# Kernel tuning notes

Hardware: AMD Instinct MI355X
Metric: run time of the kernel (lower is better)

Reference implementation:

```python
import jax, jax.numpy as jnp
import numpy as np

LN_EPS = 1e-5


def setup_inputs() -> dict:
    key = jax.random.key(0)
    ks = jax.random.split(key, 12)
    B, T, C, D, P = 4, 1024, 16, 256, 4096
    s = 1.0 / np.sqrt(D)
    x = jax.random.normal(ks[0], (B, T, C, D), jnp.float32)
    x_mask = jax.random.uniform(ks[1], (B, T, C)) < 0.1
    pos = jax.random.randint(ks[2], (B, T, C), 0, P)
    ang = jax.random.uniform(ks[3], (P, D // 2), minval=-np.pi, maxval=np.pi)
    pe = jnp.stack([jnp.cos(ang), jnp.sin(ang)], axis=-1)  # [P, D/2, 2] unit complex
    wq_w = jax.random.normal(ks[4], (D, D), jnp.float32) * s
    wq_b = jnp.zeros((D,), jnp.float32)
    wk_w = jax.random.normal(ks[5], (D, D), jnp.float32) * s
    wk_b = jnp.zeros((D,), jnp.float32)
    wv_w = jax.random.normal(ks[6], (D, D), jnp.float32) * s
    wv_b = jnp.zeros((D,), jnp.float32)
    ln_g = jnp.ones((D,), jnp.float32)
    ln_b = jnp.zeros((D,), jnp.float32)
    ls_gamma = 1e-5 * jnp.ones((D,), jnp.float32)
    return {"x": x, "x_mask": x_mask, "pos": pos, "pe": pe,
            "wq_w": wq_w, "wq_b": wq_b, "wk_w": wk_w, "wk_b": wk_b,
            "wv_w": wv_w, "wv_b": wv_b, "ln_g": ln_g, "ln_b": ln_b,
            "ls_gamma": ls_gamma}


def _rotate(q, pe, pos):
    # q: [B,T,C,D]; pe: [P,D/2,2]; pos: [B,T,C] -> complex mult q * pe[pos]
    B, T, C, D = q.shape
    qr = q.reshape(B, T, C, D // 2, 2)
    r = pe[pos]  # [B,T,C,D/2,2]
    re = qr[..., 0] * r[..., 0] - qr[..., 1] * r[..., 1]
    im = qr[..., 0] * r[..., 1] + qr[..., 1] * r[..., 0]
    return jnp.stack([re, im], axis=-1).reshape(B, T, C, D)


def reference(x, x_mask, pos, pe, wq_w, wq_b, wk_w, wk_b, wv_w, wv_b, ln_g, ln_b, ls_gamma):
    B, T, C, D = x.shape
    scale = 1.0 / jnp.sqrt(jnp.asarray(D, x.dtype))
    q = jnp.einsum('btcd,ed->btce', x, wq_w) + wq_b
    k = jnp.einsum('btcd,ed->btce', x, wk_w) + wk_b
    v = jnp.einsum('btcd,ed->btce', x, wv_w) + wv_b
    q = _rotate(q, pe, pos)
    k = _rotate(k, pe, pos)
    # (b c) t d layout -> keep as [b,c,t,d]
    q = q.transpose(0, 2, 1, 3)
    k = k.transpose(0, 2, 1, 3)
    v = v.transpose(0, 2, 1, 3)
    attn = jnp.einsum('bcqd,bckd->bcqk', q, k) * scale  # [b,c,tq,tk]
    m = x_mask.transpose(0, 2, 1)  # [b,c,t]
    mask = m[:, :, :, None] | m[:, :, None, :]  # OR-combined pad mask
    attn = jnp.where(mask, jnp.asarray(-1e30, attn.dtype), attn)
    p = jax.nn.softmax(attn, axis=-1)
    # fully masked rows: torch softmax(-inf row)->nan->nan_to_num(0)
    all_masked = jnp.all(mask, axis=-1, keepdims=True)
    p = jnp.where(all_masked, jnp.zeros((), p.dtype), p)
    o = jnp.einsum('bcqk,bckd->bqcd', p, v)  # [b,t,c,d]
    y = x + ls_gamma * o
    mu = y.mean(-1, keepdims=True)
    var = ((y - mu) ** 2).mean(-1, keepdims=True)
    out = (y - mu) / jnp.sqrt(var + LN_EPS) * ln_g + ln_b
    return out
```

## Files before the change

### kernel.cpp

```cpp
#include <hip/hip_runtime.h>


typedef __attribute__((ext_vector_type(8))) short short8_t;
typedef __attribute__((ext_vector_type(4))) short short4_t;
typedef __attribute__((ext_vector_type(8))) float float8_t;
typedef __attribute__((ext_vector_type(4))) float float4_t;
typedef __attribute__((ext_vector_type(2))) float float2_t;

__device__ __forceinline__ float b2f(short s) {
    union { unsigned int u; float f; } x;
    x.u = ((unsigned int)(unsigned short)s) << 16;
    return x.f;
}
__device__ __forceinline__ short f2bt(float f) {
    union { float f; unsigned int u; } x; x.f = f;
    return (short)(x.u >> 16);
}

__device__ __forceinline__ void stage16(const short* g, short* l) {
    __builtin_amdgcn_global_load_lds(
        (const __attribute__((address_space(1))) unsigned int*)g,
        (__attribute__((address_space(3))) unsigned int*)l, 16, 0, 0);
}

__global__ __launch_bounds__(256) void prep_kernel(
    const float* __restrict__ wq, const float* __restrict__ wk,
    const float* __restrict__ wv, const unsigned char* __restrict__ xmask,
    short* __restrict__ wb, float* __restrict__ mbg)
{
    if (blockIdx.x < 192) {
        int idx = blockIdx.x * 256 + threadIdx.x;
        int mat = idx >> 14, off = idx & 16383;
        const float* src = (mat == 0) ? wq : ((mat == 1) ? wk : wv);
        float4_t v = *(const float4_t*)(src + (long)off * 4);
        short4_t o;
#pragma unroll
        for (int j = 0; j < 4; j++) o[j] = f2bt(v[j]);
        *(short4_t*)(wb + (long)idx * 4) = o;
    } else {
        int idx = (blockIdx.x - 192) * 256 + threadIdx.x;
        int bc = idx >> 10, t = idx & 1023;
        int b = bc >> 4, c = bc & 15;
        mbg[idx] = xmask[((long)b * 1024 + t) * 16 + c] ? -1e30f : 0.0f;
    }
}

__global__ __launch_bounds__(256) void qkv_mfma_kernel(
    const float* __restrict__ x, const int* __restrict__ pos,
    const float* __restrict__ pe, const short* __restrict__ wb,
    const float* __restrict__ bq, const float* __restrict__ bk,
    const float* __restrict__ bv,
    short* __restrict__ qo, short* __restrict__ ko, short* __restrict__ vt)
{
    __shared__ __align__(16) short xs[64 * 264];
    __shared__ __align__(16) short ys[18432];
    __shared__ int posb[64];

    const int tid = threadIdx.x;
    const int lane = tid & 63;
    const int wid = tid >> 6;
    const int bc = blockIdx.x >> 4;
    const int t0 = (blockIdx.x & 15) * 64;
    const int b = bc >> 4, c = bc & 15;
    const int row = lane & 15, quad = lane >> 4;
    const int odd = lane & 1;
    const int n0 = wid * 64;
    const long kvbase = (long)bc * 262144;

#pragma unroll
    for (int j = 0; j < 8; j++) {
        int idx = tid + j * 256;
        int r = idx >> 5, c8 = idx & 31;
        const float* xp = x + (((long)b * 1024 + t0 + r) * 16 + c) * 256 + c8 * 8;
        float4_t a = *(const float4_t*)xp;
        float4_t d = *(const float4_t*)(xp + 4);
        short8_t o;
        o[0] = f2bt(a.x); o[1] = f2bt(a.y); o[2] = f2bt(a.z); o[3] = f2bt(a.w);
        o[4] = f2bt(d.x); o[5] = f2bt(d.y); o[6] = f2bt(d.z); o[7] = f2bt(d.w);
        *(short8_t*)&xs[r * 264 + c8 * 8] = o;
    }
    if (tid < 64) posb[tid] = pos[((long)b * 1024 + t0 + tid) * 16 + c];
    __syncthreads();

#pragma unroll 1
    for (int mat = 0; mat < 3; mat++) {
        const short* W = wb + mat * 65536;
        float4_t acc[4][4];
#pragma unroll
        for (int mt = 0; mt < 4; mt++)
#pragma unroll
            for (int nt = 0; nt < 4; nt++) acc[mt][nt] = (float4_t){0.f, 0.f, 0.f, 0.f};

        short8_t Ac[4], Bc[4], An[4], Bn[4];
        auto loadA = [&](short8_t* A, int k0) {
#pragma unroll
            for (int mt = 0; mt < 4; mt++)
                A[mt] = *(const short8_t*)&xs[(mt * 16 + row) * 264 + k0 * 32 + quad * 8];
        };
        auto loadB = [&](short8_t* Bf, int k0) {
#pragma unroll
            for (int nt = 0; nt < 4; nt++)
                Bf[nt] = *(const short8_t*)(W + (n0 + nt * 16 + row) * 256 + k0 * 32 + quad * 8);
        };
        loadA(Ac, 0); loadB(Bc, 0);
#pragma unroll
        for (int k0 = 0; k0 < 8; k0++) {
            if (k0 < 7) { loadA(An, k0 + 1); loadB(Bn, k0 + 1); }
#pragma unroll
            for (int mt = 0; mt < 4; mt++)
#pragma unroll
                for (int nt = 0; nt < 4; nt++)
                    acc[mt][nt] = __builtin_amdgcn_mfma_f32_16x16x32_bf16(
                        Ac[mt], Bc[nt], acc[mt][nt], 0, 0, 0);
            if (k0 < 7) {
#pragma unroll
                for (int i = 0; i < 4; i++) { Ac[i] = An[i]; Bc[i] = Bn[i]; }
            }
        }

        const float* bias = (mat == 0) ? bq : ((mat == 1) ? bk : bv);
        float bs[4];
#pragma unroll
        for (int nt = 0; nt < 4; nt++) bs[nt] = bias[n0 + nt * 16 + row];
#pragma unroll
        for (int mt = 0; mt < 4; mt++)
#pragma unroll
            for (int nt = 0; nt < 4; nt++)
#pragma unroll
                for (int r = 0; r < 4; r++) acc[mt][nt][r] += bs[nt];

        if (mat < 2) {
#pragma unroll
            for (int mt = 0; mt < 4; mt++)
#pragma unroll
                for (int r = 0; r < 4; r++) {
                    int p = posb[mt * 16 + quad * 4 + r];
                    const float* pb = pe + (long)p * 256;
#pragma unroll
                    for (int nt = 0; nt < 4; nt++) {
                        int i = (n0 + nt * 16 + row) >> 1;
                        float2_t cs = *(const float2_t*)(pb + i * 2);
                        float v = acc[mt][nt][r];
                        float pr = __shfl_xor(v, 1);
                        acc[mt][nt][r] = v * cs.x + pr * (odd ? cs.y : -cs.y);
                    }
                }
        }

        __syncthreads();
        if (mat < 2) {
#pragma unroll
            for (int mt = 0; mt < 4; mt++)
#pragma unroll
                for (int nt = 0; nt < 4; nt++) {
                    int n = n0 + nt * 16 + row;
#pragma unroll
                    for (int r = 0; r < 4; r++)
                        ys[(mt * 16 + quad * 4 + r) * 264 + n] = f2bt(acc[mt][nt][r]);
                }
            __syncthreads();
            short* dst = ((mat == 0) ? qo : ko) + kvbase + (long)t0 * 256;
#pragma unroll
            for (int j = 0; j < 8; j++) {
                int idx = tid + j * 256;
                int r = idx >> 5, c8 = idx & 31;
                *(short8_t*)(dst + r * 256 + c8 * 8) = *(const short8_t*)&ys[r * 264 + c8 * 8];
            }
        } else {
#pragma unroll
            for (int mt = 0; mt < 4; mt++)
#pragma unroll
                for (int nt = 0; nt < 4; nt++) {
                    int n = n0 + nt * 16 + row;
                    short4_t o4;
#pragma unroll
                    for (int r = 0; r < 4; r++) o4[r] = f2bt(acc[mt][nt][r]);
                    *(short4_t*)&ys[n * 72 + mt * 16 + quad * 4] = o4;
                }
            __syncthreads();
#pragma unroll
            for (int j = 0; j < 8; j++) {
                int idx = tid + j * 256;
                int d = idx >> 3, t8 = idx & 7;
                *(short8_t*)(vt + kvbase + (long)d * 1024 + t0 + t8 * 8) =
                    *(const short8_t*)&ys[d * 72 + t8 * 8];
            }
        }
    }
}

__global__ __launch_bounds__(512, 2) void attn_kernel(
    const short* __restrict__ qg, const short* __restrict__ kg,
    const short* __restrict__ vt, const float* __restrict__ mbg,
    const float* __restrict__ x,
    const float* __restrict__ lsg, const float* __restrict__ lng,
    const float* __restrict__ lnb, float* __restrict__ out)
{
    __shared__ __align__(16) short lds[72704];

    const int tid = threadIdx.x;
    const int lane = tid & 63;
    const int wid = tid >> 6;
    const int bid = (blockIdx.x & 7) * 64 + (blockIdx.x >> 3);
    const int bc = bid >> 3;
    const int tq0 = (bid & 7) * 128;
    const int b = bc >> 4, c = bc & 15;
    const long kvbase = (long)bc * 262144;
    const int bcq = bc * 1024;
    const int row = lane & 15, quad = lane >> 4;
    float* mbsf = (float*)&lds[70656];

    auto stage = [&](int j, int buf) {
#pragma unroll
        for (int i = 0; i < 2; i++) {
            int rp = (wid * 2 + i) * 2;
            int r = rp + (lane >> 5);
            int slot = lane & 31;
            const short* g = kg + kvbase + (long)(j * 32 + r) * 256 +
                             ((slot ^ (r & 7)) << 3);
            stage16(g, &lds[buf * 8192 + rp * 256]);
        }
#pragma unroll
        for (int i = 0; i < 2; i++) {
            int db = (wid * 2 + i) * 16;
            int d = db + (lane >> 2);
            int slot = lane & 3;
            const short* g = vt + kvbase + (long)d * 1024 + j * 32 +
                             (((slot ^ ((d >> 1) & 3))) << 3);
            stage16(g, &lds[32768 + buf * 8192 + db * 32]);
        }
    };

    stage(0, 0);
    stage(1, 1);
#pragma unroll
    for (int i = tid; i < 1024; i += 512) mbsf[i] = mbg[bcq + i];
    short8_t aq[8];
#pragma unroll
    for (int f = 0; f < 8; f++)
        aq[f] = *(const short8_t*)(qg + kvbase +
            (long)(tq0 + wid * 16 + row) * 256 + f * 32 + quad * 8);

    float4_t oacc[16];
#pragma unroll
    for (int nt = 0; nt < 16; nt++) oacc[nt] = (float4_t){0.f, 0.f, 0.f, 0.f};
    float m[4], lsum[4];
#pragma unroll
    for (int r = 0; r < 4; r++) { m[r] = -__builtin_inff(); lsum[r] = 0.f; }

    const float scale = 0.0625f;
    const int ptw = 65536 + wid * 640 + row * 20 + quad * 4;
    const int prd = 65536 + wid * 640 + quad * 160 + row;

    asm volatile("s_waitcnt lgkmcnt(0)" ::: "memory");

#pragma unroll 1
    for (int j = 0; j < 32; j++) {
        if (j < 30) {
            stage(j + 2, (j + 2) & 3);
            asm volatile("s_waitcnt vmcnt(8)" ::: "memory");
        } else if (j == 30) {
            asm volatile("s_waitcnt vmcnt(4)" ::: "memory");
        } else {
            asm volatile("s_waitcnt vmcnt(0)" ::: "memory");
        }
        __builtin_amdgcn_s_barrier();

        const short* Kb = &lds[(j & 3) * 8192];
        const short* Vb = &lds[32768 + (j & 3) * 8192];

        float4_t s0 = {0.f, 0.f, 0.f, 0.f}, s1 = {0.f, 0.f, 0.f, 0.f};
        __builtin_amdgcn_s_setprio(1);
#pragma unroll
        for (int f = 0; f < 8; f++) {
            short8_t k0 = *(const short8_t*)&Kb[row * 256 + (((f * 4 + quad) ^ (row & 7)) << 3)];
            short8_t k1 = *(const short8_t*)&Kb[(16 + row) * 256 + (((f * 4 + quad) ^ ((16 + row) & 7)) << 3)];
            s0 = __builtin_amdgcn_mfma_f32_16x16x32_bf16(aq[f], k0, s0, 0, 0, 0);
            s1 = __builtin_amdgcn_mfma_f32_16x16x32_bf16(aq[f], k1, s1, 0, 0, 0);
        }
        __builtin_amdgcn_s_setprio(0);
        float mb0 = mbsf[j * 32 + row], mb1 = mbsf[j * 32 + 16 + row];
        float sv[2][4], tm[4];
#pragma unroll
        for (int r = 0; r < 4; r++) {
            sv[0][r] = s0[r] * scale + mb0;
            sv[1][r] = s1[r] * scale + mb1;
            tm[r] = fmaxf(sv[0][r], sv[1][r]);
        }
#pragma unroll
        for (int r = 0; r < 4; r++)
#pragma unroll
            for (int o = 1; o < 16; o <<= 1) tm[r] = fmaxf(tm[r], __shfl_xor(tm[r], o));
        float g = fmaxf(fmaxf(tm[0] - m[0], tm[1] - m[1]),
                        fmaxf(tm[2] - m[2], tm[3] - m[3]));
        if (!__all(g <= 8.f)) {
#pragma unroll
            for (int r = 0; r < 4; r++) {
                float nm = fmaxf(m[r], tm[r]);
                float fac = __expf(m[r] - nm);
                lsum[r] *= fac; m[r] = nm;
#pragma unroll
                for (int nt = 0; nt < 16; nt++) oacc[nt][r] *= fac;
            }
        }
        short4_t p4[2];
#pragma unroll
        for (int h = 0; h < 2; h++)
#pragma unroll
            for (int r = 0; r < 4; r++) {
                float p = __expf(sv[h][r] - m[r]);
                lsum[r] += p;
                p4[h][r] = f2bt(p);
            }
        *(short4_t*)&lds[ptw] = p4[0];
        *(short4_t*)&lds[ptw + 320] = p4[1];
        short8_t pa;
#pragma unroll
        for (int jj = 0; jj < 8; jj++) pa[jj] = lds[prd + jj * 20];

        __builtin_amdgcn_s_setprio(1);
#pragma unroll
        for (int nt = 0; nt < 16; nt++) {
            int d = nt * 16 + row;
            short8_t vbf = *(const short8_t*)&Vb[d * 32 + ((quad ^ ((d >> 1) & 3)) << 3)];
            oacc[nt] = __builtin_amdgcn_mfma_f32_16x16x32_bf16(pa, vbf, oacc[nt], 0, 0, 0);
        }
        __builtin_amdgcn_s_setprio(0);
    }

    float inv[4];
#pragma unroll
    for (int r = 0; r < 4; r++) {
        float s = lsum[r];
#pragma unroll
        for (int o = 1; o < 16; o <<= 1) s += __shfl_xor(s, o);
        int qi = tq0 + wid * 16 + quad * 4 + r;
        inv[r] = (mbsf[qi] != 0.f) ? 0.f : (1.f / s);
    }
    long xb[4];
#pragma unroll
    for (int r = 0; r < 4; r++)
        xb[r] = (((long)b * 1024 + tq0 + wid * 16 + quad * 4 + r) * 16 + c) * 256 + row;

    float s1r[4] = {0.f, 0.f, 0.f, 0.f}, s2r[4] = {0.f, 0.f, 0.f, 0.f};
#pragma unroll
    for (int nt = 0; nt < 16; nt++) {
        int d = nt * 16 + row;
        float lg = lsg[d];
#pragma unroll
        for (int r = 0; r < 4; r++) {
            float yy = x[xb[r] + nt * 16] + lg * (oacc[nt][r] * inv[r]);
            oacc[nt][r] = yy;
            s1r[r] += yy; s2r[r] += yy * yy;
        }
    }
    float mu[4], rstd[4];
#pragma unroll
    for (int r = 0; r < 4; r++) {
#pragma unroll
        for (int o = 1; o < 16; o <<= 1) {
            s1r[r] += __shfl_xor(s1r[r], o);
            s2r[r] += __shfl_xor(s2r[r], o);
        }
        mu[r] = s1r[r] * (1.f / 256.f);
        float var = s2r[r] * (1.f / 256.f) - mu[r] * mu[r];
        rstd[r] = rsqrtf(var + 1e-5f);
    }
#pragma unroll
    for (int nt = 0; nt < 16; nt++) {
        int d = nt * 16 + row;
        float g2 = lng[d], b2 = lnb[d];
#pragma unroll
        for (int r = 0; r < 4; r++)
            out[xb[r] + nt * 16] = (oacc[nt][r] - mu[r]) * rstd[r] * g2 + b2;
    }
}

extern "C" void kernel_launch(void* const* d_in, const int* in_sizes, int n_in,
                              void* d_out, int out_size, void* d_ws, size_t ws_size,
                              hipStream_t stream) {
    const float* x = (const float*)d_in[0];
    const unsigned char* xmask = (const unsigned char*)d_in[1];
    const int* pos = (const int*)d_in[2];
    const float* pe = (const float*)d_in[3];
    const float* wq = (const float*)d_in[4];
    const float* bq = (const float*)d_in[5];
    const float* wk = (const float*)d_in[6];
    const float* bk = (const float*)d_in[7];
    const float* wv = (const float*)d_in[8];
    const float* bv = (const float*)d_in[9];
    const float* lng = (const float*)d_in[10];
    const float* lnb = (const float*)d_in[11];
    const float* lsg = (const float*)d_in[12];
    float* out = (float*)d_out;

    short* qw = (short*)d_ws;
    short* kw = qw + 16777216;
    short* vtw = kw + 16777216;
    short* wbw = vtw + 16777216;
    float* mbg = (float*)(wbw + 196608);

    prep_kernel<<<448, 256, 0, stream>>>(wq, wk, wv, xmask, wbw, mbg);
    qkv_mfma_kernel<<<1024, 256, 0, stream>>>(x, pos, pe, wbw, bq, bk, bv,
                                              qw, kw, vtw);
    attn_kernel<<<512, 512, 0, stream>>>(qw, kw, vtw, mbg, x, lsg, lng, lnb, out);
}
```

Before: 347.9 us.

## Switch attention to 32x32x16 MFMA with 256-query blocks and permlane P transpose

The attention kernel now gives each wave 32 query rows instead of 16 and uses 32x32x16 bf16 MFMA for both QK^T (computed transposed as K·Q) and PV. The P tile is rearranged into the A-operand layout with permlane32_swap instead of an LDS write/read round-trip, and each query's softmax state is kept per lane. Each block covers 256 queries, which halves the grid and doubles K/V reuse per LDS stage. The cost is higher register pressure (16 Q fragments and 8 float16 accumulators) and only 256 blocks, which may not fill the device at two blocks per CU.

```diff
diff --git a/kernel.cpp b/kernel.cpp
--- a/kernel.cpp
+++ b/kernel.cpp
@@ -5,7 +5,9 @@
 typedef __attribute__((ext_vector_type(4))) short short4_t;
 typedef __attribute__((ext_vector_type(8))) float float8_t;
 typedef __attribute__((ext_vector_type(4))) float float4_t;
+typedef __attribute__((ext_vector_type(16))) float float16_t;
 typedef __attribute__((ext_vector_type(2))) float float2_t;
+typedef __attribute__((ext_vector_type(2))) int int2_t;
 
 __device__ __forceinline__ float b2f(short s) {
     union { unsigned int u; float f; } x;
@@ -196,19 +198,20 @@
     const float* __restrict__ lsg, const float* __restrict__ lng,
     const float* __restrict__ lnb, float* __restrict__ out)
 {
-    __shared__ __align__(16) short lds[72704];
+    __shared__ __align__(16) short lds[68096];
 
     const int tid = threadIdx.x;
     const int lane = tid & 63;
     const int wid = tid >> 6;
-    const int bid = (blockIdx.x & 7) * 64 + (blockIdx.x >> 3);
-    const int bc = bid >> 3;
-    const int tq0 = (bid & 7) * 128;
+    const int bid = (blockIdx.x & 7) * 32 + (blockIdx.x >> 3);
+    const int bc = bid >> 2;
+    const int tq0 = (bid & 3) * 256;
     const int b = bc >> 4, c = bc & 15;
     const long kvbase = (long)bc * 262144;
     const int bcq = bc * 1024;
-    const int row = lane & 15, quad = lane >> 4;
-    float* mbsf = (float*)&lds[70656];
+    const int col = lane & 31, hi = lane >> 5;
+    float* mbsf = (float*)&lds[65536];
+    float* facb = (float*)&lds[67584];
 
     auto stage = [&](int j, int buf) {
 #pragma unroll
@@ -235,22 +238,24 @@
     stage(1, 1);
 #pragma unroll
     for (int i = tid; i < 1024; i += 512) mbsf[i] = mbg[bcq + i];
-    short8_t aq[8];
-#pragma unroll
-    for (int f = 0; f < 8; f++)
-        aq[f] = *(const short8_t*)(qg + kvbase +
-            (long)(tq0 + wid * 16 + row) * 256 + f * 32 + quad * 8);
-
-    float4_t oacc[16];
-#pragma unroll
-    for (int nt = 0; nt < 16; nt++) oacc[nt] = (float4_t){0.f, 0.f, 0.f, 0.f};
-    float m[4], lsum[4];
-#pragma unroll
-    for (int r = 0; r < 4; r++) { m[r] = -__builtin_inff(); lsum[r] = 0.f; }
+    short8_t aq[16];
+    {
+        const short* qrow = qg + kvbase + (long)(tq0 + wid * 32 + col) * 256;
+#pragma unroll
+        for (int f = 0; f < 16; f++)
+            aq[f] = *(const short8_t*)(qrow + f * 16 + hi * 8);
+    }
+
+    float16_t oacc[8];
+#pragma unroll
+    for (int nt = 0; nt < 8; nt++)
+#pragma unroll
+        for (int i = 0; i < 16; i++) oacc[nt][i] = 0.f;
+    float m = -__builtin_inff(), lsum = 0.f;
 
     const float scale = 0.0625f;
-    const int ptw = 65536 + wid * 640 + row * 20 + quad * 4;
-    const int prd = 65536 + wid * 640 + quad * 160 + row;
+    const int ksw = col & 7;
+    const int vsw = (col >> 1) & 3;
 
     asm volatile("s_waitcnt lgkmcnt(0)" ::: "memory");
 
@@ -269,110 +274,119 @@
         const short* Kb = &lds[(j & 3) * 8192];
         const short* Vb = &lds[32768 + (j & 3) * 8192];
 
-        float4_t s0 = {0.f, 0.f, 0.f, 0.f}, s1 = {0.f, 0.f, 0.f, 0.f};
+        float16_t s;
+#pragma unroll
+        for (int i = 0; i < 16; i++) s[i] = 0.f;
         __builtin_amdgcn_s_setprio(1);
 #pragma unroll
-        for (int f = 0; f < 8; f++) {
-            short8_t k0 = *(const short8_t*)&Kb[row * 256 + (((f * 4 + quad) ^ (row & 7)) << 3)];
-            short8_t k1 = *(const short8_t*)&Kb[(16 + row) * 256 + (((f * 4 + quad) ^ ((16 + row) & 7)) << 3)];
-            s0 = __builtin_amdgcn_mfma_f32_16x16x32_bf16(aq[f], k0, s0, 0, 0, 0);
-            s1 = __builtin_amdgcn_mfma_f32_16x16x32_bf16(aq[f], k1, s1, 0, 0, 0);
+        for (int f = 0; f < 16; f++) {
+            short8_t kf = *(const short8_t*)
+                &Kb[col * 256 + ((((f << 1) + hi) ^ ksw) << 3)];
+            s = __builtin_amdgcn_mfma_f32_32x32x16_bf16(kf, aq[f], s, 0, 0, 0);
         }
         __builtin_amdgcn_s_setprio(0);
-        float mb0 = mbsf[j * 32 + row], mb1 = mbsf[j * 32 + 16 + row];
-        float sv[2][4], tm[4];
-#pragma unroll
-        for (int r = 0; r < 4; r++) {
-            sv[0][r] = s0[r] * scale + mb0;
-            sv[1][r] = s1[r] * scale + mb1;
-            tm[r] = fmaxf(sv[0][r], sv[1][r]);
-        }
-#pragma unroll
-        for (int r = 0; r < 4; r++)
-#pragma unroll
-            for (int o = 1; o < 16; o <<= 1) tm[r] = fmaxf(tm[r], __shfl_xor(tm[r], o));
-        float g = fmaxf(fmaxf(tm[0] - m[0], tm[1] - m[1]),
-                        fmaxf(tm[2] - m[2], tm[3] - m[3]));
-        if (!__all(g <= 8.f)) {
-#pragma unroll
-            for (int r = 0; r < 4; r++) {
-                float nm = fmaxf(m[r], tm[r]);
-                float fac = __expf(m[r] - nm);
-                lsum[r] *= fac; m[r] = nm;
-#pragma unroll
-                for (int nt = 0; nt < 16; nt++) oacc[nt][r] *= fac;
-            }
-        }
-        short4_t p4[2];
-#pragma unroll
-        for (int h = 0; h < 2; h++)
-#pragma unroll
-            for (int r = 0; r < 4; r++) {
-                float p = __expf(sv[h][r] - m[r]);
-                lsum[r] += p;
-                p4[h][r] = f2bt(p);
-            }
-        *(short4_t*)&lds[ptw] = p4[0];
-        *(short4_t*)&lds[ptw + 320] = p4[1];
-        short8_t pa;
-#pragma unroll
-        for (int jj = 0; jj < 8; jj++) pa[jj] = lds[prd + jj * 20];
+
+        float sv[16];
+#pragma unroll
+        for (int r = 0; r < 16; r++) {
+            int kr = (r & 3) + 8 * (r >> 2) + 4 * hi;
+            sv[r] = s[r] * scale + mbsf[j * 32 + kr];
+        }
+        float tm = sv[0];
+#pragma unroll
+        for (int r = 1; r < 16; r++) tm = fmaxf(tm, sv[r]);
+        tm = fmaxf(tm, __shfl_xor(tm, 32));
+        if (!__all(tm - m <= 8.f)) {
+            float nm = fmaxf(m, tm);
+            float fac = __expf(m - nm);
+            lsum *= fac; m = nm;
+            facb[wid * 32 + col] = fac;
+            float facr[16];
+#pragma unroll
+            for (int r = 0; r < 16; r++)
+                facr[r] = facb[wid * 32 + ((r & 3) + 8 * (r >> 2) + 4 * hi)];
+#pragma unroll
+            for (int nt = 0; nt < 8; nt++)
+#pragma unroll
+                for (int r = 0; r < 16; r++) oacc[nt][r] *= facr[r];
+        }
+        float p[16];
+#pragma unroll
+        for (int r = 0; r < 16; r++) { p[r] = __expf(sv[r] - m); lsum += p[r]; }
+        unsigned int w[8];
+#pragma unroll
+        for (int i = 0; i < 8; i++)
+            w[i] = ((unsigned int)(unsigned short)f2bt(p[2 * i + 1]) << 16) |
+                   (unsigned short)f2bt(p[2 * i]);
+        int2_t q02 = __builtin_amdgcn_permlane32_swap((int)w[0], (int)w[2], false, false);
+        int2_t q13 = __builtin_amdgcn_permlane32_swap((int)w[1], (int)w[3], false, false);
+        int2_t q46 = __builtin_amdgcn_permlane32_swap((int)w[4], (int)w[6], false, false);
+        int2_t q57 = __builtin_amdgcn_permlane32_swap((int)w[5], (int)w[7], false, false);
+        short8_t pa1, pa2;
+        {
+            union { int i4[4]; short8_t s8; } u;
+            u.i4[0] = q02.x; u.i4[1] = q13.x; u.i4[2] = q02.y; u.i4[3] = q13.y;
+            pa1 = u.s8;
+            u.i4[0] = q46.x; u.i4[1] = q57.x; u.i4[2] = q46.y; u.i4[3] = q57.y;
+            pa2 = u.s8;
+        }
 
         __builtin_amdgcn_s_setprio(1);
 #pragma unroll
-        for (int nt = 0; nt < 16; nt++) {
-            int d = nt * 16 + row;
-            short8_t vbf = *(const short8_t*)&Vb[d * 32 + ((quad ^ ((d >> 1) & 3)) << 3)];
-            oacc[nt] = __builtin_amdgcn_mfma_f32_16x16x32_bf16(pa, vbf, oacc[nt], 0, 0, 0);
+        for (int nt = 0; nt < 8; nt++) {
+            const short* vp = &Vb[(nt * 32 + col) * 32];
+            short8_t v1 = *(const short8_t*)(vp + ((hi ^ vsw) << 3));
+            short8_t v2 = *(const short8_t*)(vp + (((2 + hi) ^ vsw) << 3));
+            oacc[nt] = __builtin_amdgcn_mfma_f32_32x32x16_bf16(pa1, v1, oacc[nt], 0, 0, 0);
+            oacc[nt] = __builtin_amdgcn_mfma_f32_32x32x16_bf16(pa2, v2, oacc[nt], 0, 0, 0);
         }
         __builtin_amdgcn_s_setprio(0);
     }
 
-    float inv[4];
-#pragma unroll
-    for (int r = 0; r < 4; r++) {
-        float s = lsum[r];
-#pragma unroll
-        for (int o = 1; o < 16; o <<= 1) s += __shfl_xor(s, o);
-        int qi = tq0 + wid * 16 + quad * 4 + r;
-        inv[r] = (mbsf[qi] != 0.f) ? 0.f : (1.f / s);
-    }
-    long xb[4];
-#pragma unroll
-    for (int r = 0; r < 4; r++)
-        xb[r] = (((long)b * 1024 + tq0 + wid * 16 + quad * 4 + r) * 16 + c) * 256 + row;
-
-    float s1r[4] = {0.f, 0.f, 0.f, 0.f}, s2r[4] = {0.f, 0.f, 0.f, 0.f};
-#pragma unroll
-    for (int nt = 0; nt < 16; nt++) {
-        int d = nt * 16 + row;
+    lsum += __shfl_xor(lsum, 32);
+    const int qt = tq0 + wid * 32 + col;
+    float invq = (mbsf[qt] != 0.0f) ? 0.0f : (1.0f / lsum);
+    facb[wid * 32 + col] = invq;
+    float invr[16];
+#pragma unroll
+    for (int r = 0; r < 16; r++)
+        invr[r] = facb[wid * 32 + ((r & 3) + 8 * (r >> 2) + 4 * hi)];
+
+    const long xbase = (((long)b * 1024 + tq0 + wid * 32) * 16 + c) * 256;
+    float s1r[16], s2r[16];
+#pragma unroll
+    for (int r = 0; r < 16; r++) { s1r[r] = 0.f; s2r[r] = 0.f; }
+#pragma unroll
+    for (int nt = 0; nt < 8; nt++) {
+        int d = nt * 32 + col;
         float lg = lsg[d];
 #pragma unroll
-        for (int r = 0; r < 4; r++) {
-            float yy = x[xb[r] + nt * 16] + lg * (oacc[nt][r] * inv[r]);
+        for (int r = 0; r < 16; r++) {
+            int qr = (r & 3) + 8 * (r >> 2) + 4 * hi;
+            float yy = x[xbase + (long)qr * 4096 + d] + lg * (oacc[nt][r] * invr[r]);
             oacc[nt][r] = yy;
             s1r[r] += yy; s2r[r] += yy * yy;
         }
     }
-    float mu[4], rstd[4];
-#pragma unroll
-    for (int r = 0; r < 4; r++) {
-#pragma unroll
-        for (int o = 1; o < 16; o <<= 1) {
-            s1r[r] += __shfl_xor(s1r[r], o);
-            s2r[r] += __shfl_xor(s2r[r], o);
-        }
-        mu[r] = s1r[r] * (1.f / 256.f);
-        float var = s2r[r] * (1.f / 256.f) - mu[r] * mu[r];
+    float mu[16], rstd[16];
+#pragma unroll
+    for (int r = 0; r < 16; r++) {
+        float a = s1r[r], bb = s2r[r];
+#pragma unroll
+        for (int o = 1; o < 32; o <<= 1) { a += __shfl_xor(a, o); bb += __shfl_xor(bb, o); }
+        mu[r] = a * (1.f / 256.f);
+        float var = bb * (1.f / 256.f) - mu[r] * mu[r];
         rstd[r] = rsqrtf(var + 1e-5f);
     }
 #pragma unroll
-    for (int nt = 0; nt < 16; nt++) {
-        int d = nt * 16 + row;
-        float g2 = lng[d], b2 = lnb[d];
-#pragma unroll
-        for (int r = 0; r < 4; r++)
-            out[xb[r] + nt * 16] = (oacc[nt][r] - mu[r]) * rstd[r] * g2 + b2;
+    for (int nt = 0; nt < 8; nt++) {
+        int d = nt * 32 + col;
+        float g2 = lng[d], bb = lnb[d];
+#pragma unroll
+        for (int r = 0; r < 16; r++) {
+            int qr = (r & 3) + 8 * (r >> 2) + 4 * hi;
+            out[xbase + (long)qr * 4096 + d] = (oacc[nt][r] - mu[r]) * rstd[r] * g2 + bb;
+        }
     }
 }
 
@@ -403,5 +417,5 @@
     prep_kernel<<<448, 256, 0, stream>>>(wq, wk, wv, xmask, wbw, mbg);
     qkv_mfma_kernel<<<1024, 256, 0, stream>>>(x, pos, pe, wbw, bq, bk, bv,
                                               qw, kw, vtw);
-    attn_kernel<<<512, 512, 0, stream>>>(qw, kw, vtw, mbg, x, lsg, lng, lnb, out);
-}
+    attn_kernel<<<256, 512, 0, stream>>>(qw, kw, vtw, mbg, x, lsg, lng, lnb, out);
+}
```

New measurement: 349.1 us. About the same (+0.3%).
